# Optimization experiments

Hardware: AMD Instinct MI355X
Metric: run time of the kernel (lower is better)

Reference implementation:

```python
import jax, jax.numpy as jnp
import numpy as np

N = 8192
IN_CH = 256
OUT_SZ = 64


def setup_inputs() -> dict:
    key = jax.random.key(0)
    k1, k2, k3, k4, k5 = jax.random.split(key, 5)
    x = jax.random.normal(k1, (N, IN_CH), dtype=jnp.float32)
    bias_mx = jax.random.normal(k2, (N, N), dtype=jnp.float32)
    W1 = jax.random.normal(k3, (OUT_SZ, IN_CH), dtype=jnp.float32) * (1.0 / np.sqrt(IN_CH))
    a1 = jax.random.normal(k4, (OUT_SZ,), dtype=jnp.float32) * (1.0 / np.sqrt(OUT_SZ))
    a2 = jax.random.normal(k5, (OUT_SZ,), dtype=jnp.float32) * (1.0 / np.sqrt(OUT_SZ))
    return {"x": x, "bias_mx": bias_mx, "W1": W1, "a1": a1, "a2": a2}


def reference(x, bias_mx, W1, a1, a2):
    # Conv1d(in_ch, out_sz, 1) on [1, in_ch, N] == linear projection per node
    seq_fts = x @ W1.T                        # [N, out_sz]
    f1 = seq_fts @ a1                         # [N] (conv2_1)
    f2 = seq_fts @ a2                         # [N] (conv2_2)
    # torch: logits[0, i, j] = f_1[0,0,j] + f_2[0,0,i]
    logits = f1[None, :] + f2[:, None]        # [N, N]
    logits = jax.nn.leaky_relu(logits, negative_slope=0.01)
    # torch Softmax(dim=1) on [1, N, N] -> normalize over rows (axis 0 here)
    coefs = jax.nn.softmax(logits + bias_mx, axis=0)  # [N, N]
    ret = coefs @ seq_fts                     # [N, out_sz]
    return jax.nn.elu(ret)[None]              # [1, N, out_sz]
```

## Files before the change

kernel.cpp:

```cpp
#include <hip/hip_runtime.h>
#include <hip/hip_bf16.h>

#define NN   8192
#define INCH 256
#define OUTC 64
#define LOG2E 1.44269504088896340736f

typedef __attribute__((ext_vector_type(8))) short bf16x8;
typedef __attribute__((ext_vector_type(4))) float f32x4;

static __device__ __forceinline__ unsigned short to_bf16u(float f) {
  unsigned int u = __float_as_uint(f);
  unsigned int r = u + 0x7FFFu + ((u >> 16) & 1u);
  return (unsigned short)(r >> 16);
}

__global__ __launch_bounds__(256) void k1_seqfts(
    const float* __restrict__ x, const float* __restrict__ W1,
    const float* __restrict__ a1, const float* __restrict__ a2,
    float* __restrict__ sf, float* __restrict__ f1, float* __restrict__ f2) {
  __shared__ float xs[16 * INCH];
  const int tid = threadIdx.x;
  const int i0 = blockIdx.x * 16;
  const float4* __restrict__ xg = reinterpret_cast<const float4*>(x + (size_t)i0 * INCH);
  float4* xsv = reinterpret_cast<float4*>(xs);
  #pragma unroll
  for (int idx = tid; idx < 16 * (INCH / 4); idx += 256) xsv[idx] = xg[idx];
  __syncthreads();
  const int k = tid & 63;
  const int ig = tid >> 6;
  const float4* __restrict__ wv = reinterpret_cast<const float4*>(W1 + (size_t)k * INCH);
  const float4* xr0 = reinterpret_cast<const float4*>(xs + (ig * 4 + 0) * INCH);
  const float4* xr1 = reinterpret_cast<const float4*>(xs + (ig * 4 + 1) * INCH);
  const float4* xr2 = reinterpret_cast<const float4*>(xs + (ig * 4 + 2) * INCH);
  const float4* xr3 = reinterpret_cast<const float4*>(xs + (ig * 4 + 3) * INCH);
  float acc0 = 0.f, acc1 = 0.f, acc2 = 0.f, acc3 = 0.f;
  #pragma unroll 8
  for (int c4 = 0; c4 < INCH / 4; ++c4) {
    const float4 w = wv[c4];
    float4 v;
    v = xr0[c4];
    acc0 = fmaf(w.x, v.x, acc0); acc0 = fmaf(w.y, v.y, acc0);
    acc0 = fmaf(w.z, v.z, acc0); acc0 = fmaf(w.w, v.w, acc0);
    v = xr1[c4];
    acc1 = fmaf(w.x, v.x, acc1); acc1 = fmaf(w.y, v.y, acc1);
    acc1 = fmaf(w.z, v.z, acc1); acc1 = fmaf(w.w, v.w, acc1);
    v = xr2[c4];
    acc2 = fmaf(w.x, v.x, acc2); acc2 = fmaf(w.y, v.y, acc2);
    acc2 = fmaf(w.z, v.z, acc2); acc2 = fmaf(w.w, v.w, acc2);
    v = xr3[c4];
    acc3 = fmaf(w.x, v.x, acc3); acc3 = fmaf(w.y, v.y, acc3);
    acc3 = fmaf(w.z, v.z, acc3); acc3 = fmaf(w.w, v.w, acc3);
  }
  const float A1 = a1[k], A2 = a2[k];
  #pragma unroll
  for (int r = 0; r < 4; ++r) {
    const float sv = (r == 0) ? acc0 : (r == 1) ? acc1 : (r == 2) ? acc2 : acc3;
    const int i = i0 + ig * 4 + r;
    sf[(size_t)i * OUTC + k] = sv;
    float v1 = sv * A1, v2 = sv * A2;
    #pragma unroll
    for (int m = 32; m >= 1; m >>= 1) {
      v1 += __shfl_xor(v1, m, 64);
      v2 += __shfl_xor(v2, m, 64);
    }
    if (k == 0) { f1[i] = v1; f2[i] = v2; }
  }
}

__global__ __launch_bounds__(256) void k2_colsum(
    const float* __restrict__ bias, const float* __restrict__ f1,
    const float* __restrict__ f2, float* __restrict__ Sp) {
  const int j = blockIdx.x * 1024 + threadIdx.x * 4;
  const int ibase = blockIdx.y * 64;
  const float4 F1 = *reinterpret_cast<const float4*>(f1 + j);
  float s0 = 0.f, s1 = 0.f, s2 = 0.f, s3 = 0.f;
  #pragma unroll 4
  for (int ii = 0; ii < 64; ++ii) {
    const int i = ibase + ii;
    const float fi = f2[i];
    const float4 b = *reinterpret_cast<const float4*>(bias + (size_t)i * NN + j);
    float t;
    t = F1.x + fi; t = fmaxf(t, 0.01f * t); s0 += exp2f((t + b.x) * LOG2E);
    t = F1.y + fi; t = fmaxf(t, 0.01f * t); s1 += exp2f((t + b.y) * LOG2E);
    t = F1.z + fi; t = fmaxf(t, 0.01f * t); s2 += exp2f((t + b.z) * LOG2E);
    t = F1.w + fi; t = fmaxf(t, 0.01f * t); s3 += exp2f((t + b.w) * LOG2E);
  }
  *reinterpret_cast<float4*>(Sp + (size_t)blockIdx.y * NN + j) =
      make_float4(s0, s1, s2, s3);
}

__global__ __launch_bounds__(64) void k2b_recip(
    const float* __restrict__ Sp, float* __restrict__ R) {
  const int j = blockIdx.x * 64 + threadIdx.x;
  float s = 0.f;
  #pragma unroll 8
  for (int c = 0; c < 128; ++c) s += Sp[(size_t)c * NN + j];
  R[j] = 1.0f / s;
}

__global__ __launch_bounds__(256) void k2c_transpose(
    const float* __restrict__ sf, const float* __restrict__ R,
    unsigned short* __restrict__ sT) {
  __shared__ float ls[128 * 65];
  __shared__ float Rl[128];
  const int tid = threadIdx.x;
  const int j0 = blockIdx.x * 128;
  const float4* __restrict__ sv = reinterpret_cast<const float4*>(sf + (size_t)j0 * OUTC);
  #pragma unroll
  for (int idx = tid; idx < 128 * 16; idx += 256) {
    const int row = idx >> 4, c4 = (idx & 15) * 4;
    const float4 v = sv[idx];
    float* d = ls + row * 65 + c4;
    d[0] = v.x; d[1] = v.y; d[2] = v.z; d[3] = v.w;
  }
  if (tid < 128) Rl[tid] = R[j0 + tid];
  __syncthreads();
  #pragma unroll
  for (int idx = tid; idx < OUTC * 128; idx += 256) {
    const int k = idx >> 7, jj = idx & 127;
    const float v = ls[jj * 65 + k] * Rl[jj];
    sT[(size_t)k * NN + j0 + jj] = to_bf16u(v);
  }
}

__global__ __launch_bounds__(256, 4) void k3_pv(
    const float* __restrict__ bias, const float* __restrict__ f1,
    const float* __restrict__ f2, const unsigned short* __restrict__ sT,
    float* __restrict__ retp) {
  const int tid = threadIdx.x;
  const int w = tid >> 6;
  const int l = tid & 63;
  const int lr = l & 15;
  const int lg = l >> 4;
  const int i = blockIdx.x * 64 + w * 16 + lr;
  const int jbase = blockIdx.y * 1024 + lg * 8;
  const float fi = f2[i];
  f32x4 acc0 = {0.f, 0.f, 0.f, 0.f}, acc1 = {0.f, 0.f, 0.f, 0.f};
  f32x4 acc2 = {0.f, 0.f, 0.f, 0.f}, acc3 = {0.f, 0.f, 0.f, 0.f};
  const float* __restrict__ brow = bias + (size_t)i * NN;
  const unsigned short* __restrict__ st0 = sT + (size_t)(0 * 16 + lr) * NN;
  const unsigned short* __restrict__ st1 = sT + (size_t)(1 * 16 + lr) * NN;
  const unsigned short* __restrict__ st2 = sT + (size_t)(2 * 16 + lr) * NN;
  const unsigned short* __restrict__ st3 = sT + (size_t)(3 * 16 + lr) * NN;
  #pragma unroll 2
  for (int s = 0; s < 32; ++s) {
    const int j = jbase + s * 32;
    const float4 b0 = *reinterpret_cast<const float4*>(brow + j);
    const float4 b1 = *reinterpret_cast<const float4*>(brow + j + 4);
    const float4 fa = *reinterpret_cast<const float4*>(f1 + j);
    const float4 fb = *reinterpret_cast<const float4*>(f1 + j + 4);
    float t, e0, e1, e2, e3, e4, e5, e6, e7;
    t = fa.x + fi; t = fmaxf(t, 0.01f * t); e0 = exp2f((t + b0.x) * LOG2E);
    t = fa.y + fi; t = fmaxf(t, 0.01f * t); e1 = exp2f((t + b0.y) * LOG2E);
    t = fa.z + fi; t = fmaxf(t, 0.01f * t); e2 = exp2f((t + b0.z) * LOG2E);
    t = fa.w + fi; t = fmaxf(t, 0.01f * t); e3 = exp2f((t + b0.w) * LOG2E);
    t = fb.x + fi; t = fmaxf(t, 0.01f * t); e4 = exp2f((t + b1.x) * LOG2E);
    t = fb.y + fi; t = fmaxf(t, 0.01f * t); e5 = exp2f((t + b1.y) * LOG2E);
    t = fb.z + fi; t = fmaxf(t, 0.01f * t); e6 = exp2f((t + b1.z) * LOG2E);
    t = fb.w + fi; t = fmaxf(t, 0.01f * t); e7 = exp2f((t + b1.w) * LOG2E);
    bf16x8 B;
    B[0] = (short)to_bf16u(e0); B[1] = (short)to_bf16u(e1);
    B[2] = (short)to_bf16u(e2); B[3] = (short)to_bf16u(e3);
    B[4] = (short)to_bf16u(e4); B[5] = (short)to_bf16u(e5);
    B[6] = (short)to_bf16u(e6); B[7] = (short)to_bf16u(e7);
    const bf16x8 A0 = *reinterpret_cast<const bf16x8*>(st0 + j);
    const bf16x8 A1 = *reinterpret_cast<const bf16x8*>(st1 + j);
    const bf16x8 A2 = *reinterpret_cast<const bf16x8*>(st2 + j);
    const bf16x8 A3 = *reinterpret_cast<const bf16x8*>(st3 + j);
    acc0 = __builtin_amdgcn_mfma_f32_16x16x32_bf16(A0, B, acc0, 0, 0, 0);
    acc1 = __builtin_amdgcn_mfma_f32_16x16x32_bf16(A1, B, acc1, 0, 0, 0);
    acc2 = __builtin_amdgcn_mfma_f32_16x16x32_bf16(A2, B, acc2, 0, 0, 0);
    acc3 = __builtin_amdgcn_mfma_f32_16x16x32_bf16(A3, B, acc3, 0, 0, 0);
  }
  float* __restrict__ outp =
      retp + (size_t)blockIdx.y * (NN * OUTC) + (size_t)i * OUTC;
  #pragma unroll
  for (int q = 0; q < 4; ++q) {
    outp[ 0 + lg * 4 + q] = acc0[q];
    outp[16 + lg * 4 + q] = acc1[q];
    outp[32 + lg * 4 + q] = acc2[q];
    outp[48 + lg * 4 + q] = acc3[q];
  }
}

__global__ __launch_bounds__(256) void k3b_combine(
    const float* __restrict__ retp, float* __restrict__ out) {
  const int idx = (blockIdx.x * 256 + threadIdx.x) * 4;
  float4 s = *reinterpret_cast<const float4*>(retp + idx);
  #pragma unroll
  for (int p = 1; p < 8; ++p) {
    const float4 v =
        *reinterpret_cast<const float4*>(retp + (size_t)p * (NN * OUTC) + idx);
    s.x += v.x; s.y += v.y; s.z += v.z; s.w += v.w;
  }
  s.x = (s.x > 0.f) ? s.x : expm1f(s.x);
  s.y = (s.y > 0.f) ? s.y : expm1f(s.y);
  s.z = (s.z > 0.f) ? s.z : expm1f(s.z);
  s.w = (s.w > 0.f) ? s.w : expm1f(s.w);
  *reinterpret_cast<float4*>(out + idx) = s;
}

extern "C" void kernel_launch(void* const* d_in, const int* in_sizes, int n_in,
                              void* d_out, int out_size, void* d_ws, size_t ws_size,
                              hipStream_t stream) {
  const float* x    = (const float*)d_in[0];
  const float* bias = (const float*)d_in[1];
  const float* W1   = (const float*)d_in[2];
  const float* a1   = (const float*)d_in[3];
  const float* a2   = (const float*)d_in[4];
  float* out = (float*)d_out;

  float* wsf = (float*)d_ws;
  float* f1   = wsf;
  float* f2   = wsf + 8192;
  float* R    = wsf + 16384;
  float* sf   = wsf + 24576;
  float* Sp   = wsf + 24576 + 524288;
  float* retp = wsf + 1597440;
  unsigned short* sT = (unsigned short*)(wsf + 1597440 + 4194304);

  k1_seqfts<<<512, 256, 0, stream>>>(x, W1, a1, a2, sf, f1, f2);
  k2_colsum<<<dim3(8, 128), 256, 0, stream>>>(bias, f1, f2, Sp);
  k2b_recip<<<128, 64, 0, stream>>>(Sp, R);
  k2c_transpose<<<64, 256, 0, stream>>>(sf, R, sT);
  k3_pv<<<dim3(128, 8), 256, 0, stream>>>(bias, f1, f2, sT, retp);
  k3b_combine<<<512, 256, 0, stream>>>(retp, out);
}
```

Measured before the change: 508.4 us.

## Split bias passes finer, fuse reciprocal into transpose, use native exp2

Doubles the grid of the column-sum and PV kernels by halving each block's row or column span, which gives more blocks for latency hiding on the two kernels that stream the 256MB bias matrix. It merges the reciprocal reduction into the transpose kernel, removing one launch, and caches f2 in shared memory. It also switches to the hardware exp2 builtin. The cost is more partial sums (16 PV partials and 256 column-sum partials) to reduce, which adds combine traffic.

```diff
diff --git a/kernel.cpp b/kernel.cpp
--- a/kernel.cpp
+++ b/kernel.cpp
@@ -8,6 +8,12 @@
 
 typedef __attribute__((ext_vector_type(8))) short bf16x8;
 typedef __attribute__((ext_vector_type(4))) float f32x4;
+
+#if __has_builtin(__builtin_amdgcn_exp2f)
+#define EXP2(x) __builtin_amdgcn_exp2f(x)
+#else
+#define EXP2(x) exp2f(x)
+#endif
 
 static __device__ __forceinline__ unsigned short to_bf16u(float f) {
   unsigned int u = __float_as_uint(f);
@@ -71,42 +77,47 @@
 __global__ __launch_bounds__(256) void k2_colsum(
     const float* __restrict__ bias, const float* __restrict__ f1,
     const float* __restrict__ f2, float* __restrict__ Sp) {
-  const int j = blockIdx.x * 1024 + threadIdx.x * 4;
-  const int ibase = blockIdx.y * 64;
+  __shared__ float f2s[32];
+  const int tid = threadIdx.x;
+  const int j = blockIdx.x * 1024 + tid * 4;
+  const int ibase = blockIdx.y * 32;
+  if (tid < 32) f2s[tid] = f2[ibase + tid];
+  __syncthreads();
   const float4 F1 = *reinterpret_cast<const float4*>(f1 + j);
   float s0 = 0.f, s1 = 0.f, s2 = 0.f, s3 = 0.f;
-  #pragma unroll 4
-  for (int ii = 0; ii < 64; ++ii) {
-    const int i = ibase + ii;
-    const float fi = f2[i];
-    const float4 b = *reinterpret_cast<const float4*>(bias + (size_t)i * NN + j);
+  #pragma unroll 8
+  for (int ii = 0; ii < 32; ++ii) {
+    const float fi = f2s[ii];
+    const float4 b =
+        *reinterpret_cast<const float4*>(bias + (size_t)(ibase + ii) * NN + j);
     float t;
-    t = F1.x + fi; t = fmaxf(t, 0.01f * t); s0 += exp2f((t + b.x) * LOG2E);
-    t = F1.y + fi; t = fmaxf(t, 0.01f * t); s1 += exp2f((t + b.y) * LOG2E);
-    t = F1.z + fi; t = fmaxf(t, 0.01f * t); s2 += exp2f((t + b.z) * LOG2E);
-    t = F1.w + fi; t = fmaxf(t, 0.01f * t); s3 += exp2f((t + b.w) * LOG2E);
+    t = F1.x + fi; t = fmaxf(t, 0.01f * t); s0 += EXP2((t + b.x) * LOG2E);
+    t = F1.y + fi; t = fmaxf(t, 0.01f * t); s1 += EXP2((t + b.y) * LOG2E);
+    t = F1.z + fi; t = fmaxf(t, 0.01f * t); s2 += EXP2((t + b.z) * LOG2E);
+    t = F1.w + fi; t = fmaxf(t, 0.01f * t); s3 += EXP2((t + b.w) * LOG2E);
   }
   *reinterpret_cast<float4*>(Sp + (size_t)blockIdx.y * NN + j) =
       make_float4(s0, s1, s2, s3);
 }
 
-__global__ __launch_bounds__(64) void k2b_recip(
-    const float* __restrict__ Sp, float* __restrict__ R) {
-  const int j = blockIdx.x * 64 + threadIdx.x;
-  float s = 0.f;
-  #pragma unroll 8
-  for (int c = 0; c < 128; ++c) s += Sp[(size_t)c * NN + j];
-  R[j] = 1.0f / s;
-}
-
-__global__ __launch_bounds__(256) void k2c_transpose(
-    const float* __restrict__ sf, const float* __restrict__ R,
+__global__ __launch_bounds__(256) void k2bc(
+    const float* __restrict__ Sp, const float* __restrict__ sf,
     unsigned short* __restrict__ sT) {
   __shared__ float ls[128 * 65];
   __shared__ float Rl[128];
+  __shared__ float partial[256];
   const int tid = threadIdx.x;
   const int j0 = blockIdx.x * 128;
-  const float4* __restrict__ sv = reinterpret_cast<const float4*>(sf + (size_t)j0 * OUTC);
+  const int jj = tid & 127, half = tid >> 7;
+  {
+    float s = 0.f;
+    const float* sp = Sp + (size_t)(half * 128) * NN + j0 + jj;
+    #pragma unroll 8
+    for (int c = 0; c < 128; ++c) s += sp[(size_t)c * NN];
+    partial[tid] = s;
+  }
+  const float4* __restrict__ sv =
+      reinterpret_cast<const float4*>(sf + (size_t)j0 * OUTC);
   #pragma unroll
   for (int idx = tid; idx < 128 * 16; idx += 256) {
     const int row = idx >> 4, c4 = (idx & 15) * 4;
@@ -114,13 +125,13 @@
     float* d = ls + row * 65 + c4;
     d[0] = v.x; d[1] = v.y; d[2] = v.z; d[3] = v.w;
   }
-  if (tid < 128) Rl[tid] = R[j0 + tid];
+  __syncthreads();
+  if (tid < 128) Rl[tid] = 1.0f / (partial[tid] + partial[tid + 128]);
   __syncthreads();
   #pragma unroll
   for (int idx = tid; idx < OUTC * 128; idx += 256) {
-    const int k = idx >> 7, jj = idx & 127;
-    const float v = ls[jj * 65 + k] * Rl[jj];
-    sT[(size_t)k * NN + j0 + jj] = to_bf16u(v);
+    const int k = idx >> 7, jr = idx & 127;
+    sT[(size_t)k * NN + j0 + jr] = to_bf16u(ls[jr * 65 + k] * Rl[jr]);
   }
 }
 
@@ -134,7 +145,7 @@
   const int lr = l & 15;
   const int lg = l >> 4;
   const int i = blockIdx.x * 64 + w * 16 + lr;
-  const int jbase = blockIdx.y * 1024 + lg * 8;
+  const int jbase = blockIdx.y * 512 + lg * 8;
   const float fi = f2[i];
   f32x4 acc0 = {0.f, 0.f, 0.f, 0.f}, acc1 = {0.f, 0.f, 0.f, 0.f};
   f32x4 acc2 = {0.f, 0.f, 0.f, 0.f}, acc3 = {0.f, 0.f, 0.f, 0.f};
@@ -143,22 +154,22 @@
   const unsigned short* __restrict__ st1 = sT + (size_t)(1 * 16 + lr) * NN;
   const unsigned short* __restrict__ st2 = sT + (size_t)(2 * 16 + lr) * NN;
   const unsigned short* __restrict__ st3 = sT + (size_t)(3 * 16 + lr) * NN;
-  #pragma unroll 2
-  for (int s = 0; s < 32; ++s) {
+  #pragma unroll 4
+  for (int s = 0; s < 16; ++s) {
     const int j = jbase + s * 32;
     const float4 b0 = *reinterpret_cast<const float4*>(brow + j);
     const float4 b1 = *reinterpret_cast<const float4*>(brow + j + 4);
     const float4 fa = *reinterpret_cast<const float4*>(f1 + j);
     const float4 fb = *reinterpret_cast<const float4*>(f1 + j + 4);
     float t, e0, e1, e2, e3, e4, e5, e6, e7;
-    t = fa.x + fi; t = fmaxf(t, 0.01f * t); e0 = exp2f((t + b0.x) * LOG2E);
-    t = fa.y + fi; t = fmaxf(t, 0.01f * t); e1 = exp2f((t + b0.y) * LOG2E);
-    t = fa.z + fi; t = fmaxf(t, 0.01f * t); e2 = exp2f((t + b0.z) * LOG2E);
-    t = fa.w + fi; t = fmaxf(t, 0.01f * t); e3 = exp2f((t + b0.w) * LOG2E);
-    t = fb.x + fi; t = fmaxf(t, 0.01f * t); e4 = exp2f((t + b1.x) * LOG2E);
-    t = fb.y + fi; t = fmaxf(t, 0.01f * t); e5 = exp2f((t + b1.y) * LOG2E);
-    t = fb.z + fi; t = fmaxf(t, 0.01f * t); e6 = exp2f((t + b1.z) * LOG2E);
-    t = fb.w + fi; t = fmaxf(t, 0.01f * t); e7 = exp2f((t + b1.w) * LOG2E);
+    t = fa.x + fi; t = fmaxf(t, 0.01f * t); e0 = EXP2((t + b0.x) * LOG2E);
+    t = fa.y + fi; t = fmaxf(t, 0.01f * t); e1 = EXP2((t + b0.y) * LOG2E);
+    t = fa.z + fi; t = fmaxf(t, 0.01f * t); e2 = EXP2((t + b0.z) * LOG2E);
+    t = fa.w + fi; t = fmaxf(t, 0.01f * t); e3 = EXP2((t + b0.w) * LOG2E);
+    t = fb.x + fi; t = fmaxf(t, 0.01f * t); e4 = EXP2((t + b1.x) * LOG2E);
+    t = fb.y + fi; t = fmaxf(t, 0.01f * t); e5 = EXP2((t + b1.y) * LOG2E);
+    t = fb.z + fi; t = fmaxf(t, 0.01f * t); e6 = EXP2((t + b1.z) * LOG2E);
+    t = fb.w + fi; t = fmaxf(t, 0.01f * t); e7 = EXP2((t + b1.w) * LOG2E);
     bf16x8 B;
     B[0] = (short)to_bf16u(e0); B[1] = (short)to_bf16u(e1);
     B[2] = (short)to_bf16u(e2); B[3] = (short)to_bf16u(e3);
@@ -189,7 +200,7 @@
   const int idx = (blockIdx.x * 256 + threadIdx.x) * 4;
   float4 s = *reinterpret_cast<const float4*>(retp + idx);
   #pragma unroll
-  for (int p = 1; p < 8; ++p) {
+  for (int p = 1; p < 16; ++p) {
     const float4 v =
         *reinterpret_cast<const float4*>(retp + (size_t)p * (NN * OUTC) + idx);
     s.x += v.x; s.y += v.y; s.z += v.z; s.w += v.w;
@@ -214,16 +225,15 @@
   float* wsf = (float*)d_ws;
   float* f1   = wsf;
   float* f2   = wsf + 8192;
-  float* R    = wsf + 16384;
-  float* sf   = wsf + 24576;
-  float* Sp   = wsf + 24576 + 524288;
-  float* retp = wsf + 1597440;
-  unsigned short* sT = (unsigned short*)(wsf + 1597440 + 4194304);
+  float* sf   = wsf + 16384;
+  float* Sp   = wsf + 16384 + 524288;
+  float* retp = wsf + 16384 + 524288 + 2097152;
+  unsigned short* sT =
+      (unsigned short*)(retp + 8388608);
 
   k1_seqfts<<<512, 256, 0, stream>>>(x, W1, a1, a2, sf, f1, f2);
-  k2_colsum<<<dim3(8, 128), 256, 0, stream>>>(bias, f1, f2, Sp);
-  k2b_recip<<<128, 64, 0, stream>>>(Sp, R);
-  k2c_transpose<<<64, 256, 0, stream>>>(sf, R, sT);
-  k3_pv<<<dim3(128, 8), 256, 0, stream>>>(bias, f1, f2, sT, retp);
+  k2_colsum<<<dim3(8, 256), 256, 0, stream>>>(bias, f1, f2, Sp);
+  k2bc<<<64, 256, 0, stream>>>(Sp, sf, sT);
+  k3_pv<<<dim3(128, 16), 256, 0, stream>>>(bias, f1, f2, sT, retp);
   k3b_combine<<<512, 256, 0, stream>>>(retp, out);
 }
```

After: 514.3 us. No clear change (+1.2%).
